# Kernel tuning notes

Measured on AMD Instinct MI355X. Metric: run time of the kernel, lower is better.

## Reference

```python
import jax, jax.numpy as jnp
import numpy as np

B_, L_, D_ = 8, 2048, 1024      # batch, seq_len, d_model
E, DS, K = 2, 16, 4             # expand, d_state, d_conv
DI = E * D_                     # d_inner = 2048
DTR = (D_ + 15) // 16           # dt_rank = 64


def setup_inputs() -> dict:
    key = jax.random.key(0)
    ks = jax.random.split(key, 8)
    g = lambda k, sh, sc=0.02: jax.random.normal(k, sh, jnp.float32) * sc
    return {
        "x": jax.random.normal(ks[0], (B_, L_, D_), jnp.float32),
        "ln_w": jnp.ones((D_,), jnp.float32),
        "ln_b": jnp.zeros((D_,), jnp.float32),
        "W_in": g(ks[1], (D_, 2 * DI)),
        "conv_w": g(ks[2], (DI, 1, K), 0.1),
        "conv_b": jnp.zeros((DI,), jnp.float32),
        "W_x": g(ks[3], (DI, DTR + 2 * DS)),
        "W_dt": g(ks[4], (DTR, DI), 0.1),
        "b_dt": jnp.full((DI,), -4.0, jnp.float32),  # softplus(-4) ~ 0.018 (small init dt)
        "A_log": jnp.log(jnp.broadcast_to(jnp.arange(1, DS + 1, dtype=jnp.float32), (DI, DS))),
        "Dp": jnp.ones((DI,), jnp.float32),
        "W_out": g(ks[5], (DI, D_)),
    }


def _mamba_block(x, ln_w, ln_b, W_in, conv_w, conv_b, W_x, W_dt, b_dt, A_log, Dp, W_out):
    # pre-norm
    mu = jnp.mean(x, axis=-1, keepdims=True)
    var = jnp.var(x, axis=-1, keepdims=True)
    xn = (x - mu) / jnp.sqrt(var + 1e-5) * ln_w + ln_b

    # input projection -> (u, z), each (B, L, DI)
    xz = jnp.einsum('bld,de->ble', xn, W_in)
    u, z = jnp.split(xz, 2, axis=-1)

    # causal depthwise conv1d along L
    uc = jax.lax.conv_general_dilated(
        u.transpose(0, 2, 1), conv_w, window_strides=(1,), padding=[(K - 1, 0)],
        feature_group_count=DI, dimension_numbers=('NCH', 'OIH', 'NCH'))
    u = jax.nn.silu(uc.transpose(0, 2, 1) + conv_b)

    # input-dependent SSM params
    xd = jnp.einsum('bld,de->ble', u, W_x)          # (B, L, DTR + 2*DS)
    dt = jax.nn.softplus(jnp.einsum('blr,rd->bld', xd[..., :DTR], W_dt) + b_dt)  # (B, L, DI)
    Bm = xd[..., DTR:DTR + DS]                       # (B, L, DS)
    Cm = xd[..., DTR + DS:]                          # (B, L, DS)
    A = -jnp.exp(A_log)                              # (DI, DS)

    # selective scan over time; carry h: (B, DI, DS)
    def step(h, inp):
        dt_t, u_t, B_t, C_t = inp                    # (B,DI),(B,DI),(B,DS),(B,DS)
        dA = jnp.exp(dt_t[..., None] * A)            # (B, DI, DS)
        h = h * dA + (dt_t * u_t)[..., None] * B_t[:, None, :]
        y = jnp.einsum('bds,bs->bd', h, C_t)
        return h, y

    h0 = jnp.zeros((x.shape[0], DI, DS), x.dtype)
    xs = (dt.transpose(1, 0, 2), u.transpose(1, 0, 2), Bm.transpose(1, 0, 2), Cm.transpose(1, 0, 2))
    _, ys = jax.lax.scan(step, h0, xs)               # ys: (L, B, DI)

    y = ys.transpose(1, 0, 2) + u * Dp
    y = y * jax.nn.silu(z)
    # output projection + residual (dropout is identity in eval)
    return jnp.einsum('bld,de->ble', y, W_out) + x


def reference(x, ln_w, ln_b, W_in, conv_w, conv_b, W_x, W_dt, b_dt, A_log, Dp, W_out):
    return _mamba_block(x, ln_w, ln_b, W_in, conv_w, conv_b, W_x, W_dt, b_dt, A_log, Dp, W_out)
```

## Files before the change

kernel.cpp:

```cpp
#include <hip/hip_runtime.h>

#define NB 8
#define NL 2048
#define ND 1024
#define NDI 2048
#define NDS 16
#define NDTR 64
#define NM (NB * NL)
#define CH 16
#define CL (NL / CH)

__device__ __forceinline__ float bf2f(unsigned int u) {
  union { unsigned int i; float f; } c; c.i = u << 16; return c.f;
}
__device__ __forceinline__ float lo16(unsigned int w) { return __uint_as_float(w << 16); }
__device__ __forceinline__ float hi16(unsigned int w) { return __uint_as_float(w & 0xffff0000u); }
__device__ __forceinline__ unsigned short f2bf(float f) {
  unsigned int x = __float_as_uint(f);
  x = x + 0x7fffu + ((x >> 16) & 1u);
  return (unsigned short)(x >> 16);
}
__device__ __forceinline__ void dec8(int4 raw, float* f) {
  f[0] = lo16((unsigned)raw.x); f[1] = hi16((unsigned)raw.x);
  f[2] = lo16((unsigned)raw.y); f[3] = hi16((unsigned)raw.y);
  f[4] = lo16((unsigned)raw.z); f[5] = hi16((unsigned)raw.z);
  f[6] = lo16((unsigned)raw.w); f[7] = hi16((unsigned)raw.w);
}
__device__ __forceinline__ float softplus_fast(float x) {
  return fmaxf(x, 0.f) + __logf(1.f + __expf(-fabsf(x)));
}

typedef __bf16 bf16x8 __attribute__((ext_vector_type(8)));
typedef float f32x4 __attribute__((ext_vector_type(4)));

__device__ __forceinline__ void gld_lds16(const unsigned short* g, unsigned short* l) {
  __builtin_amdgcn_global_load_lds(
      (const __attribute__((address_space(1))) unsigned int*)g,
      (__attribute__((address_space(3))) unsigned int*)l, 16, 0, 0);
}

__global__ __launch_bounds__(256) void k_ln(const float* __restrict__ x,
    const float* __restrict__ lw, const float* __restrict__ lb,
    unsigned short* __restrict__ xn)
{
  const int row = blockIdx.x;
  const int tid = threadIdx.x;
  const float* xr = x + (size_t)row * ND;
  float4 v = reinterpret_cast<const float4*>(xr)[tid];
  float s  = v.x + v.y + v.z + v.w;
  float s2 = v.x*v.x + v.y*v.y + v.z*v.z + v.w*v.w;
  #pragma unroll
  for (int m = 32; m >= 1; m >>= 1) {
    s  += __shfl_xor(s, m);
    s2 += __shfl_xor(s2, m);
  }
  __shared__ float red[8];
  const int wid = tid >> 6;
  if ((tid & 63) == 0) { red[wid] = s; red[4 + wid] = s2; }
  __syncthreads();
  s  = red[0] + red[1] + red[2] + red[3];
  s2 = red[4] + red[5] + red[6] + red[7];
  const float mu   = s * (1.0f / ND);
  const float var  = s2 * (1.0f / ND) - mu * mu;
  const float rstd = rsqrtf(var + 1e-5f);
  const float4 wv = reinterpret_cast<const float4*>(lw)[tid];
  const float4 bv = reinterpret_cast<const float4*>(lb)[tid];
  ushort4 o;
  o.x = f2bf((v.x - mu) * rstd * wv.x + bv.x);
  o.y = f2bf((v.y - mu) * rstd * wv.y + bv.y);
  o.z = f2bf((v.z - mu) * rstd * wv.z + bv.z);
  o.w = f2bf((v.w - mu) * rstd * wv.w + bv.w);
  reinterpret_cast<ushort4*>(xn + (size_t)row * ND)[tid] = o;
}

__global__ __launch_bounds__(256) void k_transpose(
    const float* __restrict__ W, unsigned short* __restrict__ WT,
    const int K, const int N)
{
  __shared__ float t[32][33];
  const int k0 = blockIdx.y * 32, n0 = blockIdx.x * 32;
  const int tx = threadIdx.x & 31, ty = threadIdx.x >> 5;
  #pragma unroll
  for (int r = 0; r < 4; ++r)
    t[ty + r * 8][tx] = W[(size_t)(k0 + ty + r * 8) * N + n0 + tx];
  __syncthreads();
  #pragma unroll
  for (int r = 0; r < 4; ++r)
    WT[(size_t)(n0 + ty + r * 8) * K + k0 + tx] = f2bf(t[tx][ty + r * 8]);
}

template<int MODE>
__global__ __launch_bounds__(512, 2) void k_mfma8(
    const unsigned short* __restrict__ A, const unsigned short* __restrict__ BT,
    const int K, const int N, void* __restrict__ O0, void* __restrict__ O1,
    const float* __restrict__ aux)
{
  __shared__ __align__(16) unsigned short sh[65536];
  const int tid = threadIdx.x, lane = tid & 63, wv = tid >> 6;
  const int wm = wv >> 2, wn = wv & 3;
  const int m16 = lane & 15, kb = lane >> 4;
  const int swzs = (((kb * 16) ^ (((m16 >> 1) & 3) << 4)) >> 1);
  const int arow = wm * 128 + m16;
  const int brow = wn * 64 + m16;

  int wg = blockIdx.x;
  const int cpx = gridDim.x >> 3;
  wg = (wg & 7) * cpx + (wg >> 3);
  const int gnx = N >> 8;
  const int m0 = (wg / gnx) << 8;
  const int n0 = (wg % gnx) << 8;

  f32x4 acc[8][4];
  #pragma unroll
  for (int i = 0; i < 8; ++i)
    #pragma unroll
    for (int j = 0; j < 4; ++j)
      #pragma unroll
      for (int r = 0; r < 4; ++r) acc[i][j][r] = 0.f;

  auto STAGE = [&](const unsigned short* X, int x0, int kg, unsigned short* base) {
    #pragma unroll
    for (int jj = 0; jj < 2; ++jj) {
      const int s = (wv * 2 + jj) * 64 + lane;
      const int row = s >> 2;
      const int c = (lane & 3) ^ ((row >> 1) & 3);
      gld_lds16(X + (size_t)(x0 + row) * K + kg + c * 8, base + (wv * 2 + jj) * 512);
    }
  };
  auto RD_A = [&](bf16x8* dst, const unsigned short* base, int FH) {
    #pragma unroll
    for (int i = 0; i < 4; ++i)
      dst[i] = *reinterpret_cast<const bf16x8*>(base + (arow + FH * 64 + i * 16) * 32 + swzs);
  };
  auto RD_B = [&](bf16x8* dst, const unsigned short* base) {
    #pragma unroll
    for (int j = 0; j < 4; ++j)
      dst[j] = *reinterpret_cast<const bf16x8*>(base + (brow + j * 16) * 32 + swzs);
  };
  auto MM = [&](const bf16x8* aF, const bf16x8* bF, int off) {
    #pragma unroll
    for (int i = 0; i < 4; ++i)
      #pragma unroll
      for (int j = 0; j < 4; ++j)
        acc[off + i][j] = __builtin_amdgcn_mfma_f32_16x16x32_bf16(aF[i], bF[j], acc[off + i][j], 0, 0, 0);
  };

  STAGE(A,  m0, 0,  sh);
  STAGE(BT, n0, 0,  sh + 32768);
  STAGE(A,  m0, 32, sh + 8192);
  STAGE(BT, n0, 32, sh + 32768 + 8192);
  asm volatile("s_waitcnt vmcnt(0)" ::: "memory");
  __builtin_amdgcn_s_barrier();

  bf16x8 aA[4], aB[4], bA[4], bB[4];
  RD_A(aA, sh, 0);
  RD_B(bA, sh + 32768);

  const int NT = K >> 6;
  for (int t = 0; t < NT; ++t) {
    const int buf = t & 1, nb = buf ^ 1;
    const int kn = (t << 6) + 64;
    const bool more = (t + 1 < NT);
    const unsigned short* cA = sh + buf * 16384;
    const unsigned short* cB = sh + 32768 + buf * 16384;
    unsigned short* nA = sh + nb * 16384;
    unsigned short* nB = sh + 32768 + nb * 16384;

    if (more) STAGE(A, m0, kn, nA);
    RD_A(aB, cA, 1);
    __builtin_amdgcn_sched_barrier(0);
    __builtin_amdgcn_s_setprio(1); MM(aA, bA, 0); __builtin_amdgcn_s_setprio(0);
    __builtin_amdgcn_s_barrier();

    if (more) STAGE(BT, n0, kn, nB);
    if (more) { asm volatile("s_waitcnt vmcnt(4)" ::: "memory"); }
    else      { asm volatile("s_waitcnt vmcnt(0)" ::: "memory"); }
    __builtin_amdgcn_s_barrier();
    RD_A(aA, cA + 8192, 0);
    RD_B(bB, cB + 8192);
    __builtin_amdgcn_sched_barrier(0);
    __builtin_amdgcn_s_setprio(1); MM(aB, bA, 4); __builtin_amdgcn_s_setprio(0);
    __builtin_amdgcn_s_barrier();

    if (more) STAGE(A, m0, kn + 32, nA + 8192);
    RD_A(aB, cA + 8192, 1);
    __builtin_amdgcn_sched_barrier(0);
    __builtin_amdgcn_s_setprio(1); MM(aA, bB, 0); __builtin_amdgcn_s_setprio(0);
    __builtin_amdgcn_s_barrier();

    if (more) STAGE(BT, n0, kn + 32, nB + 8192);
    if (more) asm volatile("s_waitcnt vmcnt(4)" ::: "memory");
    __builtin_amdgcn_s_barrier();
    if (more) { RD_A(aA, nA, 0); RD_B(bA, nB); }
    __builtin_amdgcn_sched_barrier(0);
    __builtin_amdgcn_s_setprio(1); MM(aB, bB, 4); __builtin_amdgcn_s_setprio(0);
    __builtin_amdgcn_s_barrier();
  }

  {
    float* fsh = (float*)sh;
    constexpr int LDP = 260;
    const int erow = tid >> 4;
    const int ec0  = tid & 15;
    const int growb = m0 + (erow >> 4) * 128 + (erow & 15);
    #pragma unroll
    for (int i = 0; i < 8; ++i) {
      __builtin_amdgcn_s_barrier();
      #pragma unroll
      for (int j = 0; j < 4; ++j)
        #pragma unroll
        for (int r = 0; r < 4; ++r)
          fsh[(wm * 16 + kb * 4 + r) * LDP + wn * 64 + j * 16 + m16] = acc[i][j][r];
      __builtin_amdgcn_s_barrier();
      const int grow = growb + i * 16;
      #pragma unroll
      for (int q = 0; q < 4; ++q) {
        const int c = (ec0 + q * 16) * 4;
        float4 v = *reinterpret_cast<const float4*>(&fsh[erow * LDP + c]);
        const int colg = n0 + c;
        if constexpr (MODE == 0) {
          ushort4 o = {f2bf(v.x), f2bf(v.y), f2bf(v.z), f2bf(v.w)};
          unsigned short* dst = (colg < NDI)
              ? (unsigned short*)O0 + (size_t)grow * NDI + colg
              : (unsigned short*)O1 + (size_t)grow * NDI + colg - NDI;
          *reinterpret_cast<ushort4*>(dst) = o;
        } else {
          float4 rv = *reinterpret_cast<const float4*>(aux + (size_t)grow * N + colg);
          float4 o = {v.x + rv.x, v.y + rv.y, v.z + rv.z, v.w + rv.w};
          *reinterpret_cast<float4*>((float*)O0 + (size_t)grow * N + colg) = o;
        }
      }
    }
  }
  (void)O1; (void)aux;
}

__global__ __launch_bounds__(256) void k_mfma_dt(
    const unsigned short* __restrict__ A, const unsigned short* __restrict__ BT,
    const int K, void* __restrict__ O0, const float* __restrict__ aux, const int N)
{
  __shared__ __align__(16) unsigned short As[128 * 32];
  __shared__ __align__(16) unsigned short Bs[128 * 32];
  const int tid = threadIdx.x;
  const int lane = tid & 63;
  const int wv = tid >> 6;
  const int wm = wv >> 1, wn = wv & 1;
  const int m0 = blockIdx.y * 128, n0 = blockIdx.x * 128;
  const int m16 = lane & 15, kb = lane >> 4;
  const int wbase = wv * 64;

  f32x4 acc[4][4];
  #pragma unroll
  for (int i = 0; i < 4; ++i)
    #pragma unroll
    for (int j = 0; j < 4; ++j)
      #pragma unroll
      for (int r = 0; r < 4; ++r) acc[i][j][r] = 0.f;

  for (int k0 = 0; k0 < K; k0 += 32) {
    #pragma unroll
    for (int it = 0; it < 2; ++it) {
      const int c = it * 256 + tid;
      const int r = c >> 2, cb = c & 3;
      gld_lds16(A  + (size_t)(m0 + r) * K + k0 + cb * 8, As + (size_t)(it * 256 + wbase) * 8);
      gld_lds16(BT + (size_t)(n0 + r) * K + k0 + cb * 8, Bs + (size_t)(it * 256 + wbase) * 8);
    }
    __syncthreads();
    bf16x8 af[4], bfr[4];
    #pragma unroll
    for (int i = 0; i < 4; ++i)
      af[i] = *reinterpret_cast<const bf16x8*>(&As[(wm * 64 + i * 16 + m16) * 32 + kb * 8]);
    #pragma unroll
    for (int j = 0; j < 4; ++j)
      bfr[j] = *reinterpret_cast<const bf16x8*>(&Bs[(wn * 64 + j * 16 + m16) * 32 + kb * 8]);
    #pragma unroll
    for (int i = 0; i < 4; ++i)
      #pragma unroll
      for (int j = 0; j < 4; ++j)
        acc[i][j] = __builtin_amdgcn_mfma_f32_16x16x32_bf16(af[i], bfr[j], acc[i][j], 0, 0, 0);
    __syncthreads();
  }

  const int r0 = (lane >> 4) * 4;
  #pragma unroll
  for (int i = 0; i < 4; ++i) {
    const int rowb = m0 + wm * 64 + i * 16 + r0;
    #pragma unroll
    for (int j = 0; j < 4; ++j) {
      const int col = n0 + wn * 64 + j * 16 + m16;
      #pragma unroll
      for (int r = 0; r < 4; ++r) {
        const int row = rowb + r;
        ((unsigned short*)O0)[(size_t)row * N + col] =
            f2bf(softplus_fast(acc[i][j][r] + aux[col]));
      }
    }
  }
}

__global__ __launch_bounds__(256) void k_conv(
    const unsigned short* __restrict__ up, const float* __restrict__ cw,
    const float* __restrict__ cb, unsigned short* __restrict__ u)
{
  const int tid = threadIdx.x;
  const int c0 = tid * 8;
  const int lt = blockIdx.x & 127;
  const int b  = blockIdx.x >> 7;
  const int l0 = lt * 16;

  float4 wv[8];
  #pragma unroll
  for (int j = 0; j < 8; ++j)
    wv[j] = reinterpret_cast<const float4*>(cw + (size_t)c0 * 4)[j];
  float bias[8];
  {
    float4 b0 = reinterpret_cast<const float4*>(cb + c0)[0];
    float4 b1 = reinterpret_cast<const float4*>(cb + c0)[1];
    bias[0]=b0.x; bias[1]=b0.y; bias[2]=b0.z; bias[3]=b0.w;
    bias[4]=b1.x; bias[5]=b1.y; bias[6]=b1.z; bias[7]=b1.w;
  }

  const size_t base = ((size_t)b * NL + l0) * NDI + c0;
  float w0[8], w1[8], w2[8];
  if (l0 >= 3) {
    int4 r0 = *reinterpret_cast<const int4*>(up + base - 3 * NDI);
    int4 r1 = *reinterpret_cast<const int4*>(up + base - 2 * NDI);
    int4 r2 = *reinterpret_cast<const int4*>(up + base - 1 * NDI);
    dec8(r0, w0); dec8(r1, w1); dec8(r2, w2);
  } else {
    #pragma unroll
    for (int j = 0; j < 8; ++j) { w0[j] = 0.f; w1[j] = 0.f; w2[j] = 0.f; }
  }

  #pragma unroll
  for (int l = 0; l < 16; ++l) {
    int4 raw = *reinterpret_cast<const int4*>(up + base + (size_t)l * NDI);
    float cur[8];
    dec8(raw, cur);
    unsigned short o[8];
    #pragma unroll
    for (int j = 0; j < 8; ++j) {
      const float a = bias[j] + wv[j].x * w0[j] + wv[j].y * w1[j]
                              + wv[j].z * w2[j] + wv[j].w * cur[j];
      o[j] = f2bf(a / (1.f + __expf(-a)));
    }
    ushort4 o0 = {o[0], o[1], o[2], o[3]};
    ushort4 o1 = {o[4], o[5], o[6], o[7]};
    unsigned short* dst = u + base + (size_t)l * NDI;
    *reinterpret_cast<ushort4*>(dst)     = o0;
    *reinterpret_cast<ushort4*>(dst + 4) = o1;
    #pragma unroll
    for (int j = 0; j < 8; ++j) { w0[j] = w1[j]; w1[j] = w2[j]; w2[j] = cur[j]; }
  }
}

__global__ __launch_bounds__(256) void k_xd_mfma(
    const unsigned short* __restrict__ A, const unsigned short* __restrict__ BT,
    unsigned short* __restrict__ xdt, float* __restrict__ xb,
    float* __restrict__ xc)
{
  __shared__ __align__(16) unsigned short As[128 * 32];
  __shared__ __align__(16) unsigned short Bs[96 * 32];
  const int tid = threadIdx.x, lane = tid & 63, wv = tid >> 6;
  const int m0 = blockIdx.x * 128;
  const int m16 = lane & 15, kb = lane >> 4;
  f32x4 acc[2][6];
  #pragma unroll
  for (int i = 0; i < 2; ++i)
    #pragma unroll
    for (int j = 0; j < 6; ++j)
      #pragma unroll
      for (int r = 0; r < 4; ++r) acc[i][j][r] = 0.f;

  for (int k0 = 0; k0 < NDI; k0 += 32) {
    #pragma unroll
    for (int it = 0; it < 2; ++it) {
      const int slot = it * 256 + tid;
      const int r = slot >> 2, cb = slot & 3;
      gld_lds16(A + (size_t)(m0 + r) * NDI + k0 + cb * 8, As + (size_t)slot * 8);
      if (slot < 384)
        gld_lds16(BT + (size_t)r * NDI + k0 + cb * 8, Bs + (size_t)slot * 8);
    }
    __syncthreads();
    bf16x8 af[2], bfr[6];
    #pragma unroll
    for (int i = 0; i < 2; ++i)
      af[i] = *reinterpret_cast<const bf16x8*>(&As[(wv * 32 + i * 16 + m16) * 32 + kb * 8]);
    #pragma unroll
    for (int j = 0; j < 6; ++j)
      bfr[j] = *reinterpret_cast<const bf16x8*>(&Bs[(j * 16 + m16) * 32 + kb * 8]);
    #pragma unroll
    for (int i = 0; i < 2; ++i)
      #pragma unroll
      for (int j = 0; j < 6; ++j)
        acc[i][j] = __builtin_amdgcn_mfma_f32_16x16x32_bf16(af[i], bfr[j], acc[i][j], 0, 0, 0);
    __syncthreads();
  }
  const int r0 = (lane >> 4) * 4;
  #pragma unroll
  for (int i = 0; i < 2; ++i) {
    #pragma unroll
    for (int j = 0; j < 6; ++j) {
      const int col = j * 16 + m16;
      #pragma unroll
      for (int r = 0; r < 4; ++r) {
        const int row = m0 + wv * 32 + i * 16 + r0 + r;
        const float v = acc[i][j][r];
        if (j < 4)       xdt[(size_t)row * 64 + col] = f2bf(v);
        else if (j == 4) xb[(size_t)row * 16 + col - 64] = v;
        else             xc[(size_t)row * 16 + col - 80] = v;
      }
    }
  }
}

template<int PHASE>
__global__ __launch_bounds__(256) void k_scan3(
    const unsigned short* __restrict__ dt, unsigned short* __restrict__ u_io,
    const unsigned short* __restrict__ z,
    const float* __restrict__ xb, const float* __restrict__ xc,
    const float* __restrict__ A_log, const float* __restrict__ Dp,
    float* __restrict__ HF, float* __restrict__ Sdt)
{
  const int tid = threadIdx.x;
  const int blk = blockIdx.x;
  const int b = blk >> 7;
  const int c = (blk >> 3) & (CH - 1);
  if (PHASE == 0 && c == CH - 1) return;
  const int d = (blk & 7) * 256 + tid;

  __shared__ float Bsl[CL][16];
  __shared__ float Csl[(PHASE == 1) ? CL : 1][16];
  const size_t rbase = (size_t)b * NL + (size_t)c * CL;
  #pragma unroll
  for (int i = 0; i < 2; ++i) {
    const int idx = i * 256 + tid;
    const int r = idx >> 2, q = idx & 3;
    reinterpret_cast<float4*>(&Bsl[r][q * 4])[0] =
        reinterpret_cast<const float4*>(xb + (rbase + r) * 16)[q];
    if constexpr (PHASE == 1)
      reinterpret_cast<float4*>(&Csl[r][q * 4])[0] =
          reinterpret_cast<const float4*>(xc + (rbase + r) * 16)[q];
  }
  __syncthreads();

  float Ac[16];
  #pragma unroll
  for (int q = 0; q < 4; ++q) {
    float4 a = reinterpret_cast<const float4*>(A_log + (size_t)d * 16)[q];
    Ac[q*4+0] = -__expf(a.x); Ac[q*4+1] = -__expf(a.y);
    Ac[q*4+2] = -__expf(a.z); Ac[q*4+3] = -__expf(a.w);
  }
  bool fastok = true;
  #pragma unroll
  for (int s = 1; s < 16; ++s)
    fastok = fastok && (fabsf(Ac[s] - Ac[0] * (float)(s + 1)) <= 1e-5f * fabsf(Ac[s]));
  const bool fast = __all(fastok);

  const size_t hoff = ((size_t)(b * CH + c) * NDI + d) * 16;
  float h[16];
  if constexpr (PHASE == 0) {
    #pragma unroll
    for (int s = 0; s < 16; ++s) h[s] = 0.f;
  } else {
    #pragma unroll
    for (int q = 0; q < 4; ++q) {
      float4 hv = reinterpret_cast<const float4*>(HF + hoff)[q];
      h[q*4+0] = hv.x; h[q*4+1] = hv.y; h[q*4+2] = hv.z; h[q*4+3] = hv.w;
    }
  }
  const float Dd = Dp[d];
  const float Ac0 = Ac[0];
  float sdt = 0.f;
  size_t idx = rbase * NDI + d;

  if (fast) {
    for (int l = 0; l < CL; ++l, idx += NDI) {
      const float dtv = bf2f(dt[idx]);
      const float uv  = bf2f(u_io[idx]);
      const float dtu = dtv * uv;
      const float qq = __expf(dtv * Ac0);
      float e = qq;
      if constexpr (PHASE == 0) {
        sdt += dtv;
        #pragma unroll
        for (int s = 0; s < 16; ++s) {
          h[s] = h[s] * e + dtu * Bsl[l][s];
          e *= qq;
        }
      } else {
        float yp = 0.f;
        #pragma unroll
        for (int s = 0; s < 16; ++s) {
          h[s] = h[s] * e + dtu * Bsl[l][s];
          yp += h[s] * Csl[l][s];
          e *= qq;
        }
        const float zv = bf2f(z[idx]);
        const float sil = zv / (1.f + __expf(-zv));
        u_io[idx] = f2bf((yp + uv * Dd) * sil);
      }
    }
  } else {
    for (int l = 0; l < CL; ++l, idx += NDI) {
      const float dtv = bf2f(dt[idx]);
      const float uv  = bf2f(u_io[idx]);
      const float dtu = dtv * uv;
      if constexpr (PHASE == 0) {
        sdt += dtv;
        #pragma unroll
        for (int s = 0; s < 16; ++s) {
          const float e = __expf(dtv * Ac[s]);
          h[s] = h[s] * e + dtu * Bsl[l][s];
        }
      } else {
        float yp = 0.f;
        #pragma unroll
        for (int s = 0; s < 16; ++s) {
          const float e = __expf(dtv * Ac[s]);
          h[s] = h[s] * e + dtu * Bsl[l][s];
          yp += h[s] * Csl[l][s];
        }
        const float zv = bf2f(z[idx]);
        const float sil = zv / (1.f + __expf(-zv));
        u_io[idx] = f2bf((yp + uv * Dd) * sil);
      }
    }
  }

  if constexpr (PHASE == 0) {
    #pragma unroll
    for (int q = 0; q < 4; ++q) {
      float4 hv = {h[q*4+0], h[q*4+1], h[q*4+2], h[q*4+3]};
      reinterpret_cast<float4*>(HF + hoff)[q] = hv;
    }
    Sdt[(size_t)(b * CH + c) * NDI + d] = sdt;
  }
}

__global__ __launch_bounds__(256) void k_comb(
    float* __restrict__ HF, const float* __restrict__ Sdt,
    const float* __restrict__ A_log)
{
  const int t = blockIdx.x * 256 + threadIdx.x;
  const int b = t >> 15;
  const int q = t & 32767;
  const int d = q >> 4;
  const float Ac = -__expf(A_log[q]);
  float H = 0.f;
  #pragma unroll
  for (int c = 0; c < CH; ++c) {
    const size_t off = (((size_t)(b * CH + c) * NDI) << 4) + q;
    const float hf = HF[off];
    const float p  = __expf(Ac * Sdt[(size_t)(b * CH + c) * NDI + d]);
    HF[off] = H;
    H = p * H + hf;
  }
}

extern "C" void kernel_launch(void* const* d_in, const int* in_sizes, int n_in,
                              void* d_out, int out_size, void* d_ws, size_t ws_size,
                              hipStream_t stream) {
  (void)in_sizes; (void)n_in; (void)out_size; (void)ws_size;
  const float* x      = (const float*)d_in[0];
  const float* ln_w   = (const float*)d_in[1];
  const float* ln_b   = (const float*)d_in[2];
  const float* W_in   = (const float*)d_in[3];
  const float* conv_w = (const float*)d_in[4];
  const float* conv_b = (const float*)d_in[5];
  const float* W_x    = (const float*)d_in[6];
  const float* W_dt   = (const float*)d_in[7];
  const float* b_dt   = (const float*)d_in[8];
  const float* A_log  = (const float*)d_in[9];
  const float* Dp     = (const float*)d_in[10];
  const float* W_out  = (const float*)d_in[11];
  float* out = (float*)d_out;

  char* ws = (char*)d_ws;
  unsigned short* xn   = (unsigned short*)(ws);
  float*          HF   = (float*)(ws);
  unsigned short* upre = (unsigned short*)(ws + 33554432);
  unsigned short* zbuf = (unsigned short*)(ws + 100663296);
  unsigned short* ubuf = (unsigned short*)(ws + 167772160);
  unsigned short* xdt  = (unsigned short*)(ws + 234881024);
  float*          Sdt  = (float*)(ws + 234881024);
  float*          xb   = (float*)(ws + 236978176);
  float*          xc   = (float*)(ws + 238026752);
  unsigned short* WxT  = (unsigned short*)(ws + 239075328);
  unsigned short* WdtT = (unsigned short*)(ws + 239468544);
  unsigned short* WinT = (unsigned short*)(ws + 240123904);
  unsigned short* WoutT= (unsigned short*)(ws + 248512512);

  dim3 gt1(4096 / 32, 1024 / 32);
  k_transpose<<<gt1, 256, 0, stream>>>(W_in, WinT, 1024, 4096);
  dim3 gt2(1024 / 32, 2048 / 32);
  k_transpose<<<gt2, 256, 0, stream>>>(W_out, WoutT, 2048, 1024);
  dim3 gt3(96 / 32, 2048 / 32);
  k_transpose<<<gt3, 256, 0, stream>>>(W_x, WxT, 2048, 96);
  dim3 gt4(2048 / 32, 64 / 32);
  k_transpose<<<gt4, 256, 0, stream>>>(W_dt, WdtT, 64, 2048);

  k_ln<<<NM, 256, 0, stream>>>(x, ln_w, ln_b, xn);

  k_mfma8<0><<<(NM / 256) * (4096 / 256), 512, 0, stream>>>(
      xn, WinT, 1024, 4096, upre, zbuf, nullptr);

  k_conv<<<NB * (NL / 16), 256, 0, stream>>>(upre, conv_w, conv_b, ubuf);

  k_xd_mfma<<<NM / 128, 256, 0, stream>>>(ubuf, WxT, xdt, xb, xc);

  dim3 g3(2048 / 128, NM / 128);
  k_mfma_dt<<<g3, 256, 0, stream>>>(xdt, WdtT, 64, upre, b_dt, 2048);

  const int nscan = NB * CH * (NDI / 256);
  k_scan3<0><<<nscan, 256, 0, stream>>>(upre, ubuf, zbuf, xb, xc, A_log, Dp, HF, Sdt);
  k_comb<<<NB * NDI * NDS / 256, 256, 0, stream>>>(HF, Sdt, A_log);
  k_scan3<1><<<nscan, 256, 0, stream>>>(upre, ubuf, zbuf, xb, xc, A_log, Dp, HF, Sdt);

  k_mfma8<1><<<(NM / 256) * (1024 / 256), 512, 0, stream>>>(
      ubuf, WoutT, 2048, 1024, out, nullptr, x);
}
```

Before: 546.8 us.

## Double-buffer and swizzle xd projection GEMM, halve its tile; issue GEMM loads earlier

The W_x projection kernel now uses 64-row tiles, which doubles the grid size. It double-buffers its LDS with async global-to-LDS loads and XOR-swizzles the column chunks to cut LDS bank conflicts. In the main 8-wave GEMM, both halves of the next K-tile loads are issued earlier and the waitcnt thresholds are adjusted, so more memory traffic overlaps with MFMA work. Smaller tiles reload W_x more often, and having more loads in flight raises register and queue pressure.

```diff
diff --git a/kernel.cpp b/kernel.cpp
--- a/kernel.cpp
+++ b/kernel.cpp
@@ -166,14 +166,14 @@
     unsigned short* nA = sh + nb * 16384;
     unsigned short* nB = sh + 32768 + nb * 16384;
 
-    if (more) STAGE(A, m0, kn, nA);
+    if (more) { STAGE(A, m0, kn, nA); STAGE(BT, n0, kn, nB); }
     RD_A(aB, cA, 1);
     __builtin_amdgcn_sched_barrier(0);
     __builtin_amdgcn_s_setprio(1); MM(aA, bA, 0); __builtin_amdgcn_s_setprio(0);
     __builtin_amdgcn_s_barrier();
 
-    if (more) STAGE(BT, n0, kn, nB);
-    if (more) { asm volatile("s_waitcnt vmcnt(4)" ::: "memory"); }
+    if (more) { STAGE(A, m0, kn + 32, nA + 8192); STAGE(BT, n0, kn + 32, nB + 8192); }
+    if (more) { asm volatile("s_waitcnt vmcnt(8)" ::: "memory"); }
     else      { asm volatile("s_waitcnt vmcnt(0)" ::: "memory"); }
     __builtin_amdgcn_s_barrier();
     RD_A(aA, cA + 8192, 0);
@@ -182,13 +182,11 @@
     __builtin_amdgcn_s_setprio(1); MM(aB, bA, 4); __builtin_amdgcn_s_setprio(0);
     __builtin_amdgcn_s_barrier();
 
-    if (more) STAGE(A, m0, kn + 32, nA + 8192);
     RD_A(aB, cA + 8192, 1);
     __builtin_amdgcn_sched_barrier(0);
     __builtin_amdgcn_s_setprio(1); MM(aA, bB, 0); __builtin_amdgcn_s_setprio(0);
     __builtin_amdgcn_s_barrier();
 
-    if (more) STAGE(BT, n0, kn + 32, nB + 8192);
     if (more) asm volatile("s_waitcnt vmcnt(4)" ::: "memory");
     __builtin_amdgcn_s_barrier();
     if (more) { RD_A(aA, nA, 0); RD_B(bA, nB); }
@@ -359,57 +357,64 @@
     unsigned short* __restrict__ xdt, float* __restrict__ xb,
     float* __restrict__ xc)
 {
-  __shared__ __align__(16) unsigned short As[128 * 32];
-  __shared__ __align__(16) unsigned short Bs[96 * 32];
-  const int tid = threadIdx.x, lane = tid & 63, wv = tid >> 6;
-  const int m0 = blockIdx.x * 128;
+  __shared__ __align__(16) unsigned short As[2][64 * 32];
+  __shared__ __align__(16) unsigned short Bs[2][96 * 32];
+  const int tid = threadIdx.x, lane = tid & 63, wvv = tid >> 6;
+  const int m0 = blockIdx.x * 64;
   const int m16 = lane & 15, kb = lane >> 4;
-  f32x4 acc[2][6];
-  #pragma unroll
-  for (int i = 0; i < 2; ++i)
+  const int sw = (kb ^ ((m16 >> 1) & 3)) * 8;
+
+  f32x4 acc[6];
+  #pragma unroll
+  for (int j = 0; j < 6; ++j)
+    #pragma unroll
+    for (int r = 0; r < 4; ++r) acc[j][r] = 0.f;
+
+  auto STG = [&](int bb, int kg) {
+    {
+      const int row = tid >> 2, c = tid & 3;
+      const int sc = c ^ ((row >> 1) & 3);
+      gld_lds16(A + (size_t)(m0 + row) * NDI + kg + sc * 8, &As[bb][tid * 8]);
+      gld_lds16(BT + (size_t)row * NDI + kg + sc * 8, &Bs[bb][tid * 8]);
+    }
+    if (tid < 128) {
+      const int s = 256 + tid;
+      const int row = s >> 2, c = s & 3;
+      const int sc = c ^ ((row >> 1) & 3);
+      gld_lds16(BT + (size_t)row * NDI + kg + sc * 8, &Bs[bb][s * 8]);
+    }
+  };
+
+  STG(0, 0);
+  asm volatile("s_waitcnt vmcnt(0)" ::: "memory");
+  __syncthreads();
+
+  for (int t = 0; t < NDI / 32; ++t) {
+    const int cur = t & 1;
+    if (t + 1 < NDI / 32) STG(cur ^ 1, (t + 1) * 32);
+    bf16x8 af = *reinterpret_cast<const bf16x8*>(&As[cur][(wvv * 16 + m16) * 32 + sw]);
+    bf16x8 bfr[6];
     #pragma unroll
     for (int j = 0; j < 6; ++j)
-      #pragma unroll
-      for (int r = 0; r < 4; ++r) acc[i][j][r] = 0.f;
-
-  for (int k0 = 0; k0 < NDI; k0 += 32) {
-    #pragma unroll
-    for (int it = 0; it < 2; ++it) {
-      const int slot = it * 256 + tid;
-      const int r = slot >> 2, cb = slot & 3;
-      gld_lds16(A + (size_t)(m0 + r) * NDI + k0 + cb * 8, As + (size_t)slot * 8);
-      if (slot < 384)
-        gld_lds16(BT + (size_t)r * NDI + k0 + cb * 8, Bs + (size_t)slot * 8);
-    }
+      bfr[j] = *reinterpret_cast<const bf16x8*>(&Bs[cur][(j * 16 + m16) * 32 + sw]);
+    #pragma unroll
+    for (int j = 0; j < 6; ++j)
+      acc[j] = __builtin_amdgcn_mfma_f32_16x16x32_bf16(af, bfr[j], acc[j], 0, 0, 0);
+    asm volatile("s_waitcnt vmcnt(0)" ::: "memory");
     __syncthreads();
-    bf16x8 af[2], bfr[6];
-    #pragma unroll
-    for (int i = 0; i < 2; ++i)
-      af[i] = *reinterpret_cast<const bf16x8*>(&As[(wv * 32 + i * 16 + m16) * 32 + kb * 8]);
-    #pragma unroll
-    for (int j = 0; j < 6; ++j)
-      bfr[j] = *reinterpret_cast<const bf16x8*>(&Bs[(j * 16 + m16) * 32 + kb * 8]);
-    #pragma unroll
-    for (int i = 0; i < 2; ++i)
-      #pragma unroll
-      for (int j = 0; j < 6; ++j)
-        acc[i][j] = __builtin_amdgcn_mfma_f32_16x16x32_bf16(af[i], bfr[j], acc[i][j], 0, 0, 0);
-    __syncthreads();
-  }
-  const int r0 = (lane >> 4) * 4;
-  #pragma unroll
-  for (int i = 0; i < 2; ++i) {
-    #pragma unroll
-    for (int j = 0; j < 6; ++j) {
-      const int col = j * 16 + m16;
-      #pragma unroll
-      for (int r = 0; r < 4; ++r) {
-        const int row = m0 + wv * 32 + i * 16 + r0 + r;
-        const float v = acc[i][j][r];
-        if (j < 4)       xdt[(size_t)row * 64 + col] = f2bf(v);
-        else if (j == 4) xb[(size_t)row * 16 + col - 64] = v;
-        else             xc[(size_t)row * 16 + col - 80] = v;
-      }
+  }
+
+  const int r0 = kb * 4;
+  #pragma unroll
+  for (int j = 0; j < 6; ++j) {
+    const int col = j * 16 + m16;
+    #pragma unroll
+    for (int r = 0; r < 4; ++r) {
+      const int row = m0 + wvv * 16 + r0 + r;
+      const float v = acc[j][r];
+      if (j < 4)       xdt[(size_t)row * 64 + col] = f2bf(v);
+      else if (j == 4) xb[(size_t)row * 16 + col - 64] = v;
+      else             xc[(size_t)row * 16 + col - 80] = v;
     }
   }
 }
@@ -607,7 +612,7 @@
 
   k_conv<<<NB * (NL / 16), 256, 0, stream>>>(upre, conv_w, conv_b, ubuf);
 
-  k_xd_mfma<<<NM / 128, 256, 0, stream>>>(ubuf, WxT, xdt, xb, xc);
+  k_xd_mfma<<<NM / 64, 256, 0, stream>>>(ubuf, WxT, xdt, xb, xc);
 
   dim3 g3(2048 / 128, NM / 128);
   k_mfma_dt<<<g3, 256, 0, stream>>>(xdt, WdtT, 64, upre, b_dt, 2048);
```

Measured after the change: 548.4 us. About the same (+0.3%).
